# Optimization experiments

Hardware: AMD Instinct MI355X
Metric: run time of the kernel (lower is better)

The kernel has to match this reference:

```python
import jax, jax.numpy as jnp
import numpy as np

N_CLS = 7  # only the first 7 channels contribute to the loss

def setup_inputs() -> dict:
    key = jax.random.key(0)
    k1, k2 = jax.random.split(key)
    pred = jax.random.normal(k1, (256, 16384, 8), dtype=jnp.float32)
    gt = jax.random.normal(k2, (256, 16384, 8), dtype=jnp.float32)
    return {"pred": pred, "gt": gt}

def reference(pred, gt):
    # per-batch loss: sum over objects and first 7 channels of squared error
    diff = pred[..., :N_CLS] - gt[..., :N_CLS]  # [B, N, 7]
    return jnp.sum(diff * diff, axis=(1, 2))    # [B]
```

## Files before the change

### kernel.cpp

```cpp
#include <hip/hip_runtime.h>


#define THREADS 256
#define SPLIT 8
#define F4_PER_BATCH (16384 * 2)
#define F4_PER_BLOCK (F4_PER_BATCH / SPLIT)
#define NCHUNK (F4_PER_BLOCK / THREADS)

typedef float vfloat4 __attribute__((ext_vector_type(4)));

__global__ __launch_bounds__(THREADS) void label_loss_kernel(
    const vfloat4* __restrict__ pred,
    const vfloat4* __restrict__ gt,
    float* __restrict__ out)
{
    __shared__ vfloat4 lbuf[2][2][THREADS];

    const int tid  = (int)threadIdx.x;
    const int wave = tid >> 6;
    const int b    = blockIdx.x / SPLIT;
    const int seg  = blockIdx.x % SPLIT;
    const int base_f4 = b * F4_PER_BATCH + seg * F4_PER_BLOCK + tid;

    const float m = (tid & 1) ? 0.0f : 1.0f;

#define GLD_LDS(gp_, lp_)                                                   \
    __builtin_amdgcn_global_load_lds(                                       \
        (const __attribute__((address_space(1))) unsigned*)(gp_),           \
        (__attribute__((address_space(3))) unsigned*)(lp_), 16, 0, 2)

#define STAGE(s_, c_) do {                                                  \
    const int g_ = base_f4 + (c_) * THREADS;                                \
    GLD_LDS(&pred[g_], &lbuf[s_][0][wave << 6]);                            \
    GLD_LDS(&gt[g_],   &lbuf[s_][1][wave << 6]);                            \
  } while (0)

#define WAITN(n_) do {                                                      \
    asm volatile("s_waitcnt vmcnt(" #n_ ")" ::: "memory");                  \
    __builtin_amdgcn_sched_barrier(0);                                      \
  } while (0)

    float acc = 0.0f;

#define CONSUME(s_) do {                                                    \
    const vfloat4 P_ = lbuf[s_][0][tid];                                    \
    const vfloat4 G_ = lbuf[s_][1][tid];                                    \
    const vfloat4 d_ = P_ - G_;                                             \
    acc += d_.x * d_.x + d_.y * d_.y + d_.z * d_.z + m * (d_.w * d_.w);     \
  } while (0)

    STAGE(0, 0);

    #pragma unroll
    for (int c = 0; c < NCHUNK - 1; ++c) {
        STAGE((c + 1) & 1, c + 1);
        WAITN(2);
        CONSUME(c & 1);
    }
    WAITN(0);
    CONSUME((NCHUNK - 1) & 1);

#undef STAGE
#undef WAITN
#undef CONSUME
#undef GLD_LDS

    float v = acc;

    #pragma unroll
    for (int off = 32; off > 0; off >>= 1)
        v += __shfl_down(v, off, 64);

    __shared__ float wsum[THREADS / 64];
    const int lane = tid & 63;
    if (lane == 0) wsum[wave] = v;
    __syncthreads();

    if (tid == 0) {
        atomicAdd(&out[b], wsum[0] + wsum[1] + wsum[2] + wsum[3]);
    }
}

extern "C" void kernel_launch(void* const* d_in, const int* in_sizes, int n_in,
                              void* d_out, int out_size, void* d_ws, size_t ws_size,
                              hipStream_t stream) {
    const vfloat4* pred = (const vfloat4*)d_in[0];
    const vfloat4* gt   = (const vfloat4*)d_in[1];
    float* out = (float*)d_out;

    (void)hipMemsetAsync(d_out, 0, (size_t)out_size * sizeof(float), stream);

    const int n_blocks = 256 * SPLIT;
    label_loss_kernel<<<dim3(n_blocks), dim3(THREADS), 0, stream>>>(pred, gt, out);
}
```

Measured before the change: 249.6 us.

## Load pred into registers via nontemporal loads and deepen prefetch to two chunks

```diff
diff --git a/kernel.cpp b/kernel.cpp
--- a/kernel.cpp
+++ b/kernel.cpp
@@ -6,6 +6,7 @@
 #define F4_PER_BATCH (16384 * 2)
 #define F4_PER_BLOCK (F4_PER_BATCH / SPLIT)
 #define NCHUNK (F4_PER_BLOCK / THREADS)
+#define NBUF 4
 
 typedef float vfloat4 __attribute__((ext_vector_type(4)));
 
@@ -14,7 +15,7 @@
     const vfloat4* __restrict__ gt,
     float* __restrict__ out)
 {
-    __shared__ vfloat4 lbuf[2][2][THREADS];
+    __shared__ vfloat4 lbuf[NBUF][THREADS];
 
     const int tid  = (int)threadIdx.x;
     const int wave = tid >> 6;
@@ -29,10 +30,13 @@
         (const __attribute__((address_space(1))) unsigned*)(gp_),           \
         (__attribute__((address_space(3))) unsigned*)(lp_), 16, 0, 2)
 
-#define STAGE(s_, c_) do {                                                  \
+    vfloat4 P[NBUF];
+    float acc = 0.0f;
+
+#define ISSUE(c_) do {                                                      \
     const int g_ = base_f4 + (c_) * THREADS;                                \
-    GLD_LDS(&pred[g_], &lbuf[s_][0][wave << 6]);                            \
-    GLD_LDS(&gt[g_],   &lbuf[s_][1][wave << 6]);                            \
+    P[(c_) & (NBUF - 1)] = __builtin_nontemporal_load(&pred[g_]);           \
+    GLD_LDS(&gt[g_], &lbuf[(c_) & (NBUF - 1)][wave << 6]);                  \
   } while (0)
 
 #define WAITN(n_) do {                                                      \
@@ -40,27 +44,23 @@
     __builtin_amdgcn_sched_barrier(0);                                      \
   } while (0)
 
-    float acc = 0.0f;
-
-#define CONSUME(s_) do {                                                    \
-    const vfloat4 P_ = lbuf[s_][0][tid];                                    \
-    const vfloat4 G_ = lbuf[s_][1][tid];                                    \
-    const vfloat4 d_ = P_ - G_;                                             \
+#define CONSUME(c_) do {                                                    \
+    const vfloat4 d_ = P[(c_) & (NBUF - 1)] - lbuf[(c_) & (NBUF - 1)][tid]; \
     acc += d_.x * d_.x + d_.y * d_.y + d_.z * d_.z + m * (d_.w * d_.w);     \
   } while (0)
 
-    STAGE(0, 0);
+    ISSUE(0);
+    ISSUE(1);
 
     #pragma unroll
-    for (int c = 0; c < NCHUNK - 1; ++c) {
-        STAGE((c + 1) & 1, c + 1);
-        WAITN(2);
-        CONSUME(c & 1);
+    for (int c = 0; c < NCHUNK; ++c) {
+        if (c + 2 < NCHUNK)      { ISSUE(c + 2); WAITN(4); }
+        else if (c + 1 < NCHUNK) { WAITN(2); }
+        else                     { WAITN(0); }
+        CONSUME(c);
     }
-    WAITN(0);
-    CONSUME((NCHUNK - 1) & 1);
 
-#undef STAGE
+#undef ISSUE
 #undef WAITN
 #undef CONSUME
 #undef GLD_LDS
```

New measurement: 249.7 us. About the same (+0.0%).
